# Kernel optimization log

Hardware: AMD Instinct MI355X
Metric: run time of the kernel (lower is better)

## Reference

```python
import jax, jax.numpy as jnp
import numpy as np

MAX_SEQ_LEN = 2048
H, K = 16, 8
D_IN, D_OUT = 1024, 1024
D_H, D_O = D_IN // H, D_OUT // H


def _get_phi(L, K):
    # Hankel matrix Z[i,j] = 2 / ((i+j)^3 - (i+j) + 1e-7), 1-indexed
    e = np.arange(1, L + 1, dtype=np.float64)
    s = e[:, None] + e[None, :]
    Z = 2.0 / (s ** 3 - s + 1e-7)
    sigma, phi = np.linalg.eigh(Z)
    sigma, phi = sigma[-K:], phi[:, -K:]
    phi = phi * sigma ** 0.25
    return jnp.asarray(phi, dtype=jnp.float32)  # (L, K)


def setup_inputs() -> dict:
    key = jax.random.key(0)
    k_x, k_w, k_d = jax.random.split(key, 3)
    B, T = 4, 2048
    x = jax.random.normal(k_x, (B, T, D_IN), dtype=jnp.float32)
    # kaiming_uniform(a=sqrt(5)) on (H,K,d_h,d_o): fan_in = K*d_h*d_o, bound = 1/sqrt(fan_in)
    fan_in = K * D_H * D_O
    bound = 1.0 / np.sqrt(fan_in)
    weight = jax.random.uniform(k_w, (H, K, D_H, D_O), minval=-bound, maxval=bound, dtype=jnp.float32)
    # torch init is zeros; use small random so the score path is exercised
    diag = 0.02 * jax.random.normal(k_d, (K, D_IN), dtype=jnp.float32)
    phi = _get_phi(MAX_SEQ_LEN, K)
    return {"x": x, "weight": weight, "diag": diag, "phi": phi}


def reference(x, weight, diag, phi):
    B, T, _ = x.shape
    Hh, Kk, d_h, d_o = weight.shape
    # scores: (B, T, K) = phi[:T] broadcast + x @ diag^T
    scores = phi[:T][None, :, :] + jnp.einsum('bti,ki->btk', x, diag)
    xh = x.reshape(B, T, Hh, d_h).transpose(0, 2, 1, 3)  # (B, H, T, d_h)
    # per-head, per-expert GEMM -> (B, H, K, T, d_o)
    y = jnp.einsum('bhti,hkio->bhkto', xh, weight)
    # score-weighted combine over experts -> (B, T, H, d_o)
    y = jnp.einsum('bhkto,btk->btho', y, scores)
    return y.reshape(B, T, Hh * d_o)
```

## Files before the change

### kernel.cpp

```cpp
#include <hip/hip_runtime.h>
#include <hip/hip_bf16.h>

#define BT    8192
#define SEQ_T 2048
#define DIN   1024
#define NH    16
#define NK    8
#define DH    64
#define DO    64

typedef __bf16 bf16;
typedef __attribute__((ext_vector_type(8))) __bf16 bf16x8;
typedef __attribute__((ext_vector_type(4))) __bf16 bf16x4;
typedef __attribute__((ext_vector_type(4))) float floatx4;

__global__ __launch_bounds__(256) void prep_kernel(
    const float* __restrict__ x, const float* __restrict__ weight,
    const float* __restrict__ diag, const float* __restrict__ phi,
    float* __restrict__ scores_t, bf16* __restrict__ wt, bf16* __restrict__ xh)
{
  int blk = blockIdx.x, tid = threadIdx.x;
  if (blk < BT / 4) {
    int wave = tid >> 6, lane = tid & 63;
    int token = blk * 4 + wave;
    const floatx4* xr = (const floatx4*)(x + (size_t)token * DIN);
    const floatx4* dg = (const floatx4*)diag;
    floatx4 acc[NK];
#pragma unroll
    for (int k = 0; k < NK; k++) acc[k] = (floatx4){0.f, 0.f, 0.f, 0.f};
#pragma unroll
    for (int it = 0; it < 4; it++) {
      floatx4 xv = xr[it * 64 + lane];
      int col = it * 256 + lane * 4;
      int h = col >> 6, c = col & 63;
      bf16x4 cv;
      cv[0] = (bf16)xv[0]; cv[1] = (bf16)xv[1];
      cv[2] = (bf16)xv[2]; cv[3] = (bf16)xv[3];
      *(bf16x4*)(xh + ((size_t)h * BT + token) * 64 + c) = cv;
#pragma unroll
      for (int k = 0; k < NK; k++) {
        floatx4 dv = dg[k * 256 + it * 64 + lane];
        acc[k] += xv * dv;
      }
    }
    float r[NK];
#pragma unroll
    for (int k = 0; k < NK; k++)
      r[k] = (acc[k][0] + acc[k][1]) + (acc[k][2] + acc[k][3]);
#pragma unroll
    for (int k = 0; k < NK; k++) {
      float v = r[k];
#pragma unroll
      for (int off = 32; off >= 1; off >>= 1) v += __shfl_xor(v, off, 64);
      r[k] = v;
    }
    if (lane == 0) {
      int t = token & (SEQ_T - 1);
#pragma unroll
      for (int k = 0; k < NK; k++)
        scores_t[(size_t)k * BT + token] = phi[t * NK + k] + r[k];
    }
  } else {
    __shared__ bf16 tile[64 * 68];
    int hk = blk - BT / 4;
    const float* wsrc = weight + (size_t)hk * DH * DO;
#pragma unroll
    for (int it = 0; it < 4; it++) {
      int idx = it * 1024 + tid * 4;
      int i = idx >> 6, o = idx & 63;
      floatx4 v = *(const floatx4*)(wsrc + idx);
#pragma unroll
      for (int r = 0; r < 4; r++)
        tile[(o + r) * 68 + i] = (bf16)v[r];
    }
    __syncthreads();
#pragma unroll
    for (int it = 0; it < 4; it++) {
      int idx = it * 1024 + tid * 4;
      int o2 = idx >> 6, i2 = idx & 63;
      bf16x4 v = *(const bf16x4*)&tile[o2 * 68 + i2];
      *(bf16x4*)(wt + (size_t)hk * 4096 + idx) = v;
    }
  }
}

__global__ __launch_bounds__(256, 3) void moe_kernel(
    const bf16* __restrict__ xh, const bf16* __restrict__ wt,
    const float* __restrict__ scores_t, float* __restrict__ out)
{
  __shared__ bf16  xl[128 * 64];
  __shared__ bf16  wl[256 * 64];
  __shared__ float sl[NK * 128];

  int bid = blockIdx.x;
  int g  = bid >> 5;
  int h  = (bid >> 1) & 15;
  int nh = bid & 1;
  int tid = threadIdx.x, lane = tid & 63, w = tid >> 6;
  int l15 = lane & 15, q = lane >> 4;

  {
    const bf16* xs = xh + ((size_t)h * BT + g * 128) * 64;
#pragma unroll
    for (int it = 0; it < 4; it++) {
      int idx = it * 256 + tid;
      int row = idx >> 3, c = idx & 7, pc = c ^ (row & 7);
      bf16x8 v = *(const bf16x8*)(xs + idx * 8);
      *(bf16x8*)(xl + row * 64 + pc * 8) = v;
    }
  }
  {
#pragma unroll
    for (int it = 0; it < 8; it++) {
      int idx = it * 256 + tid;
      int R = idx >> 3, c = idx & 7;
      int e = R >> 5, o = R & 31;
      bf16x8 v = *(const bf16x8*)(wt + ((size_t)(h * NK + e) * DO + nh * 32 + o) * 64 + c * 8);
      int pc = c ^ (R & 7);
      *(bf16x8*)(wl + R * 64 + pc * 8) = v;
    }
  }
  {
    int k = tid >> 5, t4 = (tid & 31) * 4;
    floatx4 v = *(const floatx4*)(scores_t + (size_t)k * BT + g * 128 + t4);
    *(floatx4*)(sl + k * 128 + t4) = v;
  }
  __syncthreads();

  int mh = w >> 1;
  int ns = w & 1;

  bf16x8 b[NK][2];
#pragma unroll
  for (int e = 0; e < NK; e++) {
    int R = e * 32 + ns * 16 + l15;
#pragma unroll
    for (int ki = 0; ki < 2; ki++) {
      int pc = (ki * 4 + q) ^ (R & 7);
      b[e][ki] = *(const bf16x8*)(wl + R * 64 + pc * 8);
    }
  }

#pragma unroll
  for (int m = 0; m < 4; m++) {
    int tr = mh * 64 + m * 16;
    int row = tr + l15;
    int p0 = q ^ (row & 7), p1 = (q + 4) ^ (row & 7);
    bf16x8 a0 = *(const bf16x8*)(xl + row * 64 + p0 * 8);
    bf16x8 a1 = *(const bf16x8*)(xl + row * 64 + p1 * 8);
    floatx4 y = (floatx4){0.f, 0.f, 0.f, 0.f};
#pragma unroll
    for (int e = 0; e < NK; e++) {
      floatx4 s4 = *(const floatx4*)(sl + e * 128 + tr + q * 4);
      floatx4 z = (floatx4){0.f, 0.f, 0.f, 0.f};
      z = __builtin_amdgcn_mfma_f32_16x16x32_bf16(a0, b[e][0], z, 0, 0, 0);
      z = __builtin_amdgcn_mfma_f32_16x16x32_bf16(a1, b[e][1], z, 0, 0, 0);
      y += s4 * z;
    }
    int orow = g * 128 + tr + q * 4;
    float* op = out + (size_t)orow * (NH * DO) + h * DO + nh * 32 + ns * 16 + l15;
#pragma unroll
    for (int r = 0; r < 4; r++)
      op[(size_t)r * (NH * DO)] = y[r];
  }
}

extern "C" void kernel_launch(void* const* d_in, const int* in_sizes, int n_in,
                              void* d_out, int out_size, void* d_ws, size_t ws_size,
                              hipStream_t stream) {
  const float* x      = (const float*)d_in[0];
  const float* weight = (const float*)d_in[1];
  const float* diag   = (const float*)d_in[2];
  const float* phi    = (const float*)d_in[3];
  float* out = (float*)d_out;

  bf16*  wt       = (bf16*)d_ws;
  float* scores_t = (float*)((char*)d_ws + (2u << 20));
  bf16*  xh       = (bf16*)((char*)d_ws + (4u << 20));

  prep_kernel<<<BT / 4 + NH * NK, 256, 0, stream>>>(x, weight, diag, phi,
                                                    scores_t, wt, xh);
  moe_kernel<<<64 * NH * 2, 256, 0, stream>>>(xh, wt, scores_t, out);
}
```

Measured before the change: 108.9 us.

## Drop bf16 x staging buffer; convert x in MoE kernel with double-buffered tiles

The prep kernel no longer writes a head-major bf16 copy of x. It computes scores for four tokens per wave, so each diag load is reused across those tokens. The MoE kernel now reads fp32 x directly, converts it to bf16 into a double-buffered LDS tile, and prefetches the next 128-token group while computing the current one. Each block keeps its weight slice resident across four token groups. This removes the intermediate xh round-trip through global memory. In exchange the grid is smaller (512 blocks at occupancy 2), the fp32 x reads are strided per head, and scores are read from global memory rather than LDS.

```diff
diff --git a/kernel.cpp b/kernel.cpp
--- a/kernel.cpp
+++ b/kernel.cpp
@@ -17,52 +17,54 @@
 __global__ __launch_bounds__(256) void prep_kernel(
     const float* __restrict__ x, const float* __restrict__ weight,
     const float* __restrict__ diag, const float* __restrict__ phi,
-    float* __restrict__ scores_t, bf16* __restrict__ wt, bf16* __restrict__ xh)
+    float* __restrict__ scores_t, bf16* __restrict__ wt)
 {
   int blk = blockIdx.x, tid = threadIdx.x;
-  if (blk < BT / 4) {
+  if (blk < BT / 16) {
     int wave = tid >> 6, lane = tid & 63;
-    int token = blk * 4 + wave;
-    const floatx4* xr = (const floatx4*)(x + (size_t)token * DIN);
+    int tok = blk * 16 + wave * 4;
     const floatx4* dg = (const floatx4*)diag;
-    floatx4 acc[NK];
-#pragma unroll
-    for (int k = 0; k < NK; k++) acc[k] = (floatx4){0.f, 0.f, 0.f, 0.f};
+    float acc[4][NK];
+#pragma unroll
+    for (int j = 0; j < 4; j++)
+#pragma unroll
+      for (int k = 0; k < NK; k++) acc[j][k] = 0.f;
 #pragma unroll
     for (int it = 0; it < 4; it++) {
-      floatx4 xv = xr[it * 64 + lane];
-      int col = it * 256 + lane * 4;
-      int h = col >> 6, c = col & 63;
-      bf16x4 cv;
-      cv[0] = (bf16)xv[0]; cv[1] = (bf16)xv[1];
-      cv[2] = (bf16)xv[2]; cv[3] = (bf16)xv[3];
-      *(bf16x4*)(xh + ((size_t)h * BT + token) * 64 + c) = cv;
+      floatx4 xv[4];
+#pragma unroll
+      for (int j = 0; j < 4; j++)
+        xv[j] = ((const floatx4*)(x + (size_t)(tok + j) * DIN))[it * 64 + lane];
 #pragma unroll
       for (int k = 0; k < NK; k++) {
         floatx4 dv = dg[k * 256 + it * 64 + lane];
-        acc[k] += xv * dv;
-      }
-    }
-    float r[NK];
-#pragma unroll
-    for (int k = 0; k < NK; k++)
-      r[k] = (acc[k][0] + acc[k][1]) + (acc[k][2] + acc[k][3]);
-#pragma unroll
-    for (int k = 0; k < NK; k++) {
-      float v = r[k];
-#pragma unroll
-      for (int off = 32; off >= 1; off >>= 1) v += __shfl_xor(v, off, 64);
-      r[k] = v;
-    }
+#pragma unroll
+        for (int j = 0; j < 4; j++)
+          acc[j][k] = fmaf(xv[j][0], dv[0], fmaf(xv[j][1], dv[1],
+                      fmaf(xv[j][2], dv[2], fmaf(xv[j][3], dv[3], acc[j][k]))));
+      }
+    }
+#pragma unroll
+    for (int j = 0; j < 4; j++)
+#pragma unroll
+      for (int k = 0; k < NK; k++) {
+        float v = acc[j][k];
+#pragma unroll
+        for (int off = 32; off >= 1; off >>= 1) v += __shfl_xor(v, off, 64);
+        acc[j][k] = v;
+      }
     if (lane == 0) {
-      int t = token & (SEQ_T - 1);
-#pragma unroll
-      for (int k = 0; k < NK; k++)
-        scores_t[(size_t)k * BT + token] = phi[t * NK + k] + r[k];
+#pragma unroll
+      for (int j = 0; j < 4; j++) {
+        int t = (tok + j) & (SEQ_T - 1);
+#pragma unroll
+        for (int k = 0; k < NK; k++)
+          scores_t[(size_t)k * BT + tok + j] = phi[t * NK + k] + acc[j][k];
+      }
     }
   } else {
     __shared__ bf16 tile[64 * 68];
-    int hk = blk - BT / 4;
+    int hk = blk - BT / 16;
     const float* wsrc = weight + (size_t)hk * DH * DO;
 #pragma unroll
     for (int it = 0; it < 4; it++) {
@@ -84,84 +86,111 @@
   }
 }
 
-__global__ __launch_bounds__(256, 3) void moe_kernel(
-    const bf16* __restrict__ xh, const bf16* __restrict__ wt,
+__global__ __launch_bounds__(256, 2) void moe_kernel(
+    const float* __restrict__ x, const bf16* __restrict__ wt,
     const float* __restrict__ scores_t, float* __restrict__ out)
 {
-  __shared__ bf16  xl[128 * 64];
-  __shared__ bf16  wl[256 * 64];
-  __shared__ float sl[NK * 128];
+  __shared__ bf16 wl[256 * 64];
+  __shared__ bf16 xl[2][128 * 64];
 
   int bid = blockIdx.x;
-  int g  = bid >> 5;
-  int h  = (bid >> 1) & 15;
-  int nh = bid & 1;
+  int h    = bid >> 5;
+  int nh   = (bid >> 4) & 1;
+  int slot = bid & 15;
   int tid = threadIdx.x, lane = tid & 63, w = tid >> 6;
   int l15 = lane & 15, q = lane >> 4;
+  int mh = w >> 1, ns = w & 1;
 
   {
-    const bf16* xs = xh + ((size_t)h * BT + g * 128) * 64;
-#pragma unroll
-    for (int it = 0; it < 4; it++) {
-      int idx = it * 256 + tid;
-      int row = idx >> 3, c = idx & 7, pc = c ^ (row & 7);
-      bf16x8 v = *(const bf16x8*)(xs + idx * 8);
-      *(bf16x8*)(xl + row * 64 + pc * 8) = v;
-    }
-  }
-  {
+    const bf16* wh = wt + ((size_t)h * NK * DO + nh * 32) * DH;
 #pragma unroll
     for (int it = 0; it < 8; it++) {
       int idx = it * 256 + tid;
       int R = idx >> 3, c = idx & 7;
       int e = R >> 5, o = R & 31;
-      bf16x8 v = *(const bf16x8*)(wt + ((size_t)(h * NK + e) * DO + nh * 32 + o) * 64 + c * 8);
-      int pc = c ^ (R & 7);
-      *(bf16x8*)(wl + R * 64 + pc * 8) = v;
-    }
-  }
+      bf16x8 v = *(const bf16x8*)(wh + (size_t)e * DO * DH + o * 64 + c * 8);
+      *(bf16x8*)(wl + R * 64 + (c ^ (R & 7)) * 8) = v;
+    }
+  }
+
+  const float* xc = x + (size_t)h * DH;
+  int g0 = slot * 4;
+
+  floatx4 xv[8];
   {
-    int k = tid >> 5, t4 = (tid & 31) * 4;
-    floatx4 v = *(const floatx4*)(scores_t + (size_t)k * BT + g * 128 + t4);
-    *(floatx4*)(sl + k * 128 + t4) = v;
+    const float* base = xc + (size_t)(g0 * 128) * DIN;
+#pragma unroll
+    for (int j = 0; j < 8; j++) {
+      int f = j * 1024 + tid * 4;
+      xv[j] = *(const floatx4*)(base + (size_t)(f >> 6) * DIN + (f & 63));
+    }
+  }
+#pragma unroll
+  for (int j = 0; j < 8; j++) {
+    int f = j * 1024 + tid * 4;
+    int row = f >> 6, col = f & 63;
+    bf16x4 c4;
+    c4[0] = (bf16)xv[j][0]; c4[1] = (bf16)xv[j][1];
+    c4[2] = (bf16)xv[j][2]; c4[3] = (bf16)xv[j][3];
+    *(bf16x4*)(&xl[0][0] + row * 64 + ((col >> 3) ^ (row & 7)) * 8 + (col & 7)) = c4;
   }
   __syncthreads();
-
-  int mh = w >> 1;
-  int ns = w & 1;
 
   bf16x8 b[NK][2];
 #pragma unroll
   for (int e = 0; e < NK; e++) {
     int R = e * 32 + ns * 16 + l15;
 #pragma unroll
-    for (int ki = 0; ki < 2; ki++) {
-      int pc = (ki * 4 + q) ^ (R & 7);
-      b[e][ki] = *(const bf16x8*)(wl + R * 64 + pc * 8);
-    }
-  }
-
-#pragma unroll
-  for (int m = 0; m < 4; m++) {
-    int tr = mh * 64 + m * 16;
-    int row = tr + l15;
-    int p0 = q ^ (row & 7), p1 = (q + 4) ^ (row & 7);
-    bf16x8 a0 = *(const bf16x8*)(xl + row * 64 + p0 * 8);
-    bf16x8 a1 = *(const bf16x8*)(xl + row * 64 + p1 * 8);
-    floatx4 y = (floatx4){0.f, 0.f, 0.f, 0.f};
-#pragma unroll
-    for (int e = 0; e < NK; e++) {
-      floatx4 s4 = *(const floatx4*)(sl + e * 128 + tr + q * 4);
-      floatx4 z = (floatx4){0.f, 0.f, 0.f, 0.f};
-      z = __builtin_amdgcn_mfma_f32_16x16x32_bf16(a0, b[e][0], z, 0, 0, 0);
-      z = __builtin_amdgcn_mfma_f32_16x16x32_bf16(a1, b[e][1], z, 0, 0, 0);
-      y += s4 * z;
-    }
-    int orow = g * 128 + tr + q * 4;
-    float* op = out + (size_t)orow * (NH * DO) + h * DO + nh * 32 + ns * 16 + l15;
-#pragma unroll
-    for (int r = 0; r < 4; r++)
-      op[(size_t)r * (NH * DO)] = y[r];
+    for (int ki = 0; ki < 2; ki++)
+      b[e][ki] = *(const bf16x8*)(wl + R * 64 + ((ki * 4 + q) ^ (R & 7)) * 8);
+  }
+
+#pragma unroll
+  for (int i = 0; i < 4; i++) {
+    int g = g0 + i;
+    if (i < 3) {
+      const float* base = xc + (size_t)((g + 1) * 128) * DIN;
+#pragma unroll
+      for (int j = 0; j < 8; j++) {
+        int f = j * 1024 + tid * 4;
+        xv[j] = *(const floatx4*)(base + (size_t)(f >> 6) * DIN + (f & 63));
+      }
+    }
+    const bf16* xb = &xl[i & 1][0];
+#pragma unroll
+    for (int m = 0; m < 4; m++) {
+      int row = mh * 64 + m * 16 + l15;
+      bf16x8 a0 = *(const bf16x8*)(xb + row * 64 + ((q    ) ^ (row & 7)) * 8);
+      bf16x8 a1 = *(const bf16x8*)(xb + row * 64 + ((q + 4) ^ (row & 7)) * 8);
+      floatx4 y = (floatx4){0.f, 0.f, 0.f, 0.f};
+      int sbase = g * 128 + mh * 64 + m * 16 + q * 4;
+#pragma unroll
+      for (int e = 0; e < NK; e++) {
+        floatx4 s4 = *(const floatx4*)(scores_t + (size_t)e * BT + sbase);
+        floatx4 z = (floatx4){0.f, 0.f, 0.f, 0.f};
+        z = __builtin_amdgcn_mfma_f32_16x16x32_bf16(a0, b[e][0], z, 0, 0, 0);
+        z = __builtin_amdgcn_mfma_f32_16x16x32_bf16(a1, b[e][1], z, 0, 0, 0);
+        y += s4 * z;
+      }
+      float* op = out + (size_t)(g * 128 + mh * 64 + m * 16 + q * 4) * (NH * DO)
+                      + h * DO + nh * 32 + ns * 16 + l15;
+#pragma unroll
+      for (int r = 0; r < 4; r++)
+        op[(size_t)r * (NH * DO)] = y[r];
+    }
+    if (i < 3) {
+      bf16* xn = &xl[(i + 1) & 1][0];
+#pragma unroll
+      for (int j = 0; j < 8; j++) {
+        int f = j * 1024 + tid * 4;
+        int row = f >> 6, col = f & 63;
+        bf16x4 c4;
+        c4[0] = (bf16)xv[j][0]; c4[1] = (bf16)xv[j][1];
+        c4[2] = (bf16)xv[j][2]; c4[3] = (bf16)xv[j][3];
+        *(bf16x4*)(xn + row * 64 + ((col >> 3) ^ (row & 7)) * 8 + (col & 7)) = c4;
+      }
+      __syncthreads();
+    }
   }
 }
 
@@ -176,9 +205,8 @@
 
   bf16*  wt       = (bf16*)d_ws;
   float* scores_t = (float*)((char*)d_ws + (2u << 20));
-  bf16*  xh       = (bf16*)((char*)d_ws + (4u << 20));
-
-  prep_kernel<<<BT / 4 + NH * NK, 256, 0, stream>>>(x, weight, diag, phi,
-                                                    scores_t, wt, xh);
-  moe_kernel<<<64 * NH * 2, 256, 0, stream>>>(xh, wt, scores_t, out);
+
+  prep_kernel<<<BT / 16 + NH * NK, 256, 0, stream>>>(x, weight, diag, phi,
+                                                     scores_t, wt);
+  moe_kernel<<<NH * 2 * 16, 256, 0, stream>>>(x, wt, scores_t, out);
 }
```

Measured after the change: 111.0 us. Within noise of the previous version (+2.0%).
